# Optimization experiments

Hardware: AMD Instinct MI355X
Metric: run time of the kernel (lower is better)

Reference implementation:

```python
import jax, jax.numpy as jnp
import numpy as np

NUM_CODES = 8192
DIM = 256
TAU = 1.0
KL_WEIGHT = 0.01
COMMIT_WEIGHT = 0.25
B, C, P = 8, 64, 32


def setup_inputs() -> dict:
    key = jax.random.key(0)
    kz, kc = jax.random.split(key)
    z = jax.random.normal(kz, (B, C, P, DIM), dtype=jnp.float32)
    # nn.init.normal_(codebook.weight, std=1/sqrt(dim))
    codebook = jax.random.normal(kc, (NUM_CODES, DIM), dtype=jnp.float32) / jnp.sqrt(jnp.float32(DIM))
    return {"z": z, "codebook": codebook}


def reference(z, codebook):
    Bq, Cq, Pq, D = z.shape
    flat = z.reshape(-1, D)                                  # (N, D)
    logits = flat @ codebook.T                               # (N, num_codes)
    # training path: gumbel-softmax (hard=False), fixed key for determinism
    g = jax.random.gumbel(jax.random.key(42), logits.shape, dtype=logits.dtype)
    soft_one_hot = jax.nn.softmax((logits + g) / TAU, axis=-1)
    z_q = (soft_one_hot @ codebook).reshape(Bq, Cq, Pq, D)
    # KL to uniform prior: sum(qy * log(qy * K + 1e-10))
    log_qy = jax.nn.log_softmax(logits, axis=-1)
    qy = jnp.exp(log_qy)
    kl_loss = KL_WEIGHT * jnp.mean(jnp.sum(qy * jnp.log(qy * NUM_CODES + 1e-10), axis=-1))
    codes = jnp.argmax(logits, axis=-1).reshape(Bq, Cq, Pq)
    commit_loss = COMMIT_WEIGHT * jnp.mean((jax.lax.stop_gradient(z_q) - z) ** 2)
    z_q_st = z + jax.lax.stop_gradient(z_q - z)              # straight-through
    total_loss = commit_loss + kl_loss
    return (z_q_st, total_loss, codes)
```

## Files before the change

kernel.cpp:

```cpp
#include <hip/hip_runtime.h>
#include <stdint.h>
#include <math.h>

#define N_ROWS   16384
#define N_CODES  8192
#define DIMV     256
#define RT       32
#define CK       32
#define NCHUNK   (N_CODES / CK)
#define OUT_ZQ_N ((size_t)N_ROWS * DIMV)
#define OUT_LOSS OUT_ZQ_N
#define OUT_CODE (OUT_ZQ_N + 1)

#define WS_CBHI 0u
#define WS_CBT  4194304u
#define WS_ACC  8388608u
#define WS_NEED (8388608u + 64u)

#define CB1H_OFF  0
#define CBT_OFF   16896
#define BSTRIDE   1056
#define P_OFF     33792
#define P_ROW     80
#define S2B_OFF   36352
#define SKL_OFF   36608
#define TKL_OFF   36864
#define SMEM_BYTES 37120
#define ZT_ROWF   260
#define CAND_OFF  0

typedef __attribute__((ext_vector_type(8))) short short8;
typedef __attribute__((ext_vector_type(4))) float float4v;

typedef __attribute__((address_space(1))) uint32_t g_u32;
typedef __attribute__((address_space(3))) uint32_t l_u32;

__device__ __forceinline__ void dma16(const void* gsrc, void* ldst) {
  __builtin_amdgcn_global_load_lds((g_u32*)gsrc, (l_u32*)ldst, 16, 0, 0);
}

__device__ __forceinline__ uint32_t rotl32(uint32_t x, int r) {
  return __builtin_rotateleft32(x, (uint32_t)r);
}

__device__ __forceinline__ uint32_t threefry_bits(uint32_t c) {
  const uint32_t k0 = 0u, k1 = 42u;
  const uint32_t k2 = 0x1BD11BDAu ^ k0 ^ k1;
  uint32_t x0 = 0u + k0;
  uint32_t x1 = c + k1;
#define TF_R(r) { x0 += x1; x1 = rotl32(x1, r); x1 ^= x0; }
  TF_R(13) TF_R(15) TF_R(26) TF_R(6)
  x0 += k1; x1 += k2 + 1u;
  TF_R(17) TF_R(29) TF_R(16) TF_R(24)
  x0 += k2; x1 += k0 + 2u;
  TF_R(13) TF_R(15) TF_R(26) TF_R(6)
  x0 += k0; x1 += k1 + 3u;
  TF_R(17) TF_R(29) TF_R(16) TF_R(24)
  x0 += k1; x1 += k2 + 4u;
  TF_R(13) TF_R(15) TF_R(26) TF_R(6)
  x0 += k2; x1 += k0 + 5u;
#undef TF_R
  return x0 ^ x1;
}

__device__ __forceinline__ float gumbel_at_v1(uint32_t idx) {
  uint32_t bits = threefry_bits(idx);
  float u = __uint_as_float((bits >> 9) | 0x3f800000u) - 1.0f;
  u = fmaxf(u, 1.17549435e-38f);
  return -logf(-logf(u));
}

__device__ __forceinline__ unsigned short f2bf(float x) {
  uint32_t u = __float_as_uint(x);
  u += 0x7fffu + ((u >> 16) & 1u);
  return (unsigned short)(u >> 16);
}
__device__ __forceinline__ float bf2f(unsigned short h) {
  return __uint_as_float(((uint32_t)h) << 16);
}

__global__ __launch_bounds__(256)
void vq_prep(const float* __restrict__ cb, char* __restrict__ ws) {
  __shared__ unsigned short lhs[32 * 260];
  const int c = blockIdx.x;
  const int tid = threadIdx.x;
  const int k0 = c * 32;
  unsigned short* cbhi = (unsigned short*)(ws + WS_CBHI);
  unsigned short* cbt  = (unsigned short*)(ws + WS_CBT);
#pragma unroll
  for (int i = 0; i < 8; ++i) {
    int F = tid + i * 256;
    int code = F >> 6, d4 = (F & 63) * 4;
    float4 v = *(const float4*)(cb + (size_t)(k0 + code) * DIMV + d4);
    unsigned short h0 = f2bf(v.x), h1 = f2bf(v.y), h2 = f2bf(v.z), h3 = f2bf(v.w);
    ushort4 hv = {h0, h1, h2, h3};
    *(ushort4*)(cbhi + (size_t)(k0 + code) * DIMV + d4) = hv;
    *(ushort4*)(&lhs[code * 260 + d4]) = hv;
  }
  __syncthreads();
  const int d = tid;
  unsigned short vals[32];
#pragma unroll
  for (int cc = 0; cc < 32; ++cc) vals[cc] = lhs[cc * 260 + d];
  unsigned short* base = cbt + (size_t)c * 8192 + (size_t)d * 32;
#pragma unroll
  for (int j = 0; j < 8; ++j) {
    ushort4 w = {vals[4 * j], vals[4 * j + 1], vals[4 * j + 2], vals[4 * j + 3]};
    *(ushort4*)(base + j * 4) = w;
  }
}

__global__ __launch_bounds__(256, 4)
void vq_main_v2(const float* __restrict__ z, const float* __restrict__ cb,
                float* __restrict__ out, char* __restrict__ ws) {
  __shared__ __align__(16) char sm[SMEM_BYTES];
  const int tid  = threadIdx.x;
  const int wave = tid >> 6;
  const int lane = tid & 63;
  const int quad = lane >> 4;
  const int n    = lane & 15;
  const int mt   = wave & 1;
  const int nt   = wave >> 1;
  const int r0   = blockIdx.x * RT;
  const int myrow = mt * 16 + quad * 4;
  const char* cbhi_b = ws + WS_CBHI;
  const char* cbt_b  = ws + WS_CBT;
  float* wsA = (float*)(ws + WS_ACC);

  {
    float* zts = (float*)sm;
#pragma unroll
    for (int i = 0; i < 8; ++i) {
      int F = tid + i * 256;
      int row = F >> 6, d4 = (F & 63) * 4;
      *(float4*)(zts + row * ZT_ROWF + d4) =
          *(const float4*)(z + (size_t)(r0 + row) * DIMV + d4);
    }
  }
  __syncthreads();
  short8 zhi[8];
  {
    const float* zts = (const float*)sm;
    const int rowl = mt * 16 + n;
#pragma unroll
    for (int ks = 0; ks < 8; ++ks) {
      const float* zp = zts + rowl * ZT_ROWF + ks * 32 + quad * 8;
      float4 f0 = *(const float4*)zp;
      float4 f1 = *(const float4*)(zp + 4);
      zhi[ks][0] = (short)f2bf(f0.x); zhi[ks][1] = (short)f2bf(f0.y);
      zhi[ks][2] = (short)f2bf(f0.z); zhi[ks][3] = (short)f2bf(f0.w);
      zhi[ks][4] = (short)f2bf(f1.x); zhi[ks][5] = (short)f2bf(f1.y);
      zhi[ks][6] = (short)f2bf(f1.z); zhi[ks][7] = (short)f2bf(f1.w);
    }
  }
  __syncthreads();

#pragma unroll
  for (int i = 0; i < 4; ++i) {
    int b = wave * 4 + i;
    dma16(cbhi_b + (size_t)(2 * b) * 512 + (size_t)lane * 16, sm + CB1H_OFF + b * BSTRIDE);
  }

  float skl[4] = {0.f, 0.f, 0.f, 0.f};
  float tkl[4] = {0.f, 0.f, 0.f, 0.f};
  float s2l[4] = {0.f, 0.f, 0.f, 0.f};
  float v1[4], v2[4];
  int   i1[4], i2[4];
  uint32_t idxr[4];
#pragma unroll
  for (int r = 0; r < 4; ++r) {
    v1[r] = -INFINITY; v2[r] = -INFINITY;
    i1[r] = 0x7fffffff; i2[r] = 0x7fffffff;
    idxr[r] = (uint32_t)(r0 + myrow + r) * (uint32_t)N_CODES + (uint32_t)(nt * 16 + n);
  }
  float4v acc2[8];
#pragma unroll
  for (int t = 0; t < 8; ++t) acc2[t] = (float4v){0.f, 0.f, 0.f, 0.f};

  const int kc = nt * 16 + n;
  const char* bbase = sm + CB1H_OFF + (kc >> 1) * BSTRIDE + (kc & 1) * 512 + quad * 16;

  for (int c = 0; c < NCHUNK; ++c) {
    __syncthreads();

#pragma unroll
    for (int i = 0; i < 4; ++i) {
      int b = wave * 4 + i;
      dma16(cbt_b + (size_t)c * 16384 + (size_t)b * 1024 + (size_t)lane * 16,
            sm + CBT_OFF + b * BSTRIDE);
    }

    float4v e0 = (float4v){0.f, 0.f, 0.f, 0.f};
    float4v e1 = (float4v){0.f, 0.f, 0.f, 0.f};
#pragma unroll
    for (int ks = 0; ks < 4; ++ks) {
      short8 ba = *(const short8*)(bbase + (2 * ks) * 64);
      short8 bb = *(const short8*)(bbase + (2 * ks + 1) * 64);
      e0 = __builtin_amdgcn_mfma_f32_16x16x32_bf16(zhi[2 * ks], ba, e0, 0, 0, 0);
      e1 = __builtin_amdgcn_mfma_f32_16x16x32_bf16(zhi[2 * ks + 1], bb, e1, 0, 0, 0);
    }
    float4v acc1 = e0 + e1;

    const int codeg0 = c * CK + kc;
#pragma unroll
    for (int r = 0; r < 4; ++r) {
      float l = acc1[r];
      uint32_t bits = threefry_bits(idxr[r]);
      idxr[r] += 32u;
      float u = __uint_as_float((bits >> 9) | 0x3f800000u) - 1.0f;
      float t = -0.69314718056f * __log2f(fmaxf(u, 1.17549435e-38f));
      t = fmaxf(t, 1.0e-10f);
      float e = __expf(l);
      skl[r] += e;
      tkl[r] = fmaf(e, l, tkl[r]);
      bool b1 = l > v1[r];
      bool b2 = l > v2[r];
      v2[r] = b1 ? v1[r] : (b2 ? l : v2[r]);
      i2[r] = b1 ? i1[r] : (b2 ? codeg0 : i2[r]);
      v1[r] = b1 ? l : v1[r];
      i1[r] = b1 ? codeg0 : i1[r];
      float p = e * __builtin_amdgcn_rcpf(t) * 6.1442123533282097e-06f;
      unsigned short ph = f2bf(p);
      s2l[r] += bf2f(ph);
      *(unsigned short*)(sm + P_OFF + (myrow + r) * P_ROW + kc * 2) = ph;
    }
    __syncthreads();

    if (c + 1 < NCHUNK) {
      const size_t k1 = (size_t)(c + 1) * CK;
#pragma unroll
      for (int i = 0; i < 4; ++i) {
        int b = wave * 4 + i;
        dma16(cbhi_b + (k1 + 2 * b) * 512 + (size_t)lane * 16, sm + CB1H_OFF + b * BSTRIDE);
      }
    }

    {
      short8 pah0 = *(const short8*)(sm + P_OFF + n * P_ROW + quad * 16);
      short8 pah1 = *(const short8*)(sm + P_OFF + (16 + n) * P_ROW + quad * 16);
#pragma unroll
      for (int t = 0; t < 4; ++t) {
        int dt = wave * 4 + t;
        short8 bb = *(const short8*)(sm + CBT_OFF + dt * BSTRIDE + n * 64 + quad * 16);
        acc2[t * 2 + 0] = __builtin_amdgcn_mfma_f32_16x16x32_bf16(pah0, bb, acc2[t * 2 + 0], 0, 0, 0);
        acc2[t * 2 + 1] = __builtin_amdgcn_mfma_f32_16x16x32_bf16(pah1, bb, acc2[t * 2 + 1], 0, 0, 0);
      }
    }
  }

#pragma unroll
  for (int m = 1; m <= 8; m <<= 1) {
#pragma unroll
    for (int r = 0; r < 4; ++r) {
      s2l[r] += __shfl_xor(s2l[r], m);
      skl[r] += __shfl_xor(skl[r], m);
      tkl[r] += __shfl_xor(tkl[r], m);
    }
  }
  if (n == 0) {
    int off = (nt * 32 + myrow) * 4;
    float4 fs = {s2l[0], s2l[1], s2l[2], s2l[3]};
    *(float4*)(sm + S2B_OFF + off) = fs;
    float4 fk = {skl[0], skl[1], skl[2], skl[3]};
    *(float4*)(sm + SKL_OFF + off) = fk;
    float4 ft = {tkl[0], tkl[1], tkl[2], tkl[3]};
    *(float4*)(sm + TKL_OFF + off) = ft;
  }
#pragma unroll
  for (int r = 0; r < 4; ++r) {
    char* cbase = sm + CAND_OFF + (myrow + r) * 512 + (nt * 32 + n * 2) * 8;
    *(float*)(cbase + 0) = v1[r];
    *(int*)(cbase + 4)   = i1[r];
    *(float*)(cbase + 8) = v2[r];
    *(int*)(cbase + 12)  = i2[r];
  }
  __syncthreads();

  if (tid < 32) {
    int r = tid;
    const float* sklb = (const float*)(sm + SKL_OFF);
    const float* tklb = (const float*)(sm + TKL_OFF);
    float S = sklb[r] + sklb[32 + r];
    float T = tklb[r] + tklb[32 + r];
    float klr = T / S - __logf(S) + 9.010913347279288f;
#pragma unroll
    for (int m = 1; m <= 16; m <<= 1) klr += __shfl_xor(klr, m);
    if (r == 0) atomicAdd(&wsA[0], klr);
  }

  if (tid < 64) {
    int r = tid >> 1, h = tid & 1;
    const char* cbase = sm + CAND_OFF + r * 512 + h * 256;
    float bv[8]; int bi8[8];
#pragma unroll
    for (int k = 0; k < 8; ++k) { bv[k] = -INFINITY; bi8[k] = 0x7fffffff; }
    for (int s = 0; s < 32; ++s) {
      float v = *(const float*)(cbase + s * 8);
      int  id = *(const int*)(cbase + s * 8 + 4);
      if ((v > bv[7]) || (v == bv[7] && id < bi8[7])) {
        float cv = v; int ci = id;
#pragma unroll
        for (int k = 0; k < 8; ++k) {
          bool sw = (cv > bv[k]) || (cv == bv[k] && ci < bi8[k]);
          float tv = bv[k]; int ti = bi8[k];
          if (sw) { bv[k] = cv; bi8[k] = ci; cv = tv; ci = ti; }
        }
      }
    }
    float ovv[8]; int ovi[8];
#pragma unroll
    for (int k = 0; k < 8; ++k) {
      ovv[k] = __shfl_xor(bv[k], 1);
      ovi[k] = __shfl_xor(bi8[k], 1);
    }
#pragma unroll
    for (int kk = 0; kk < 8; ++kk) {
      float cv = ovv[kk]; int ci = ovi[kk];
      if ((cv > bv[7]) || (cv == bv[7] && ci < bi8[7])) {
#pragma unroll
        for (int k = 0; k < 8; ++k) {
          bool sw = (cv > bv[k]) || (cv == bv[k] && ci < bi8[k]);
          float tv = bv[k]; int ti = bi8[k];
          if (sw) { bv[k] = cv; bi8[k] = ci; cv = tv; ci = ti; }
        }
      }
    }
    const float* zp = z + (size_t)(r0 + r) * DIMV;
    double best = -1.0e300;
    int bidx = 0x7fffffff;
#pragma unroll
    for (int k = 0; k < 4; ++k) {
      int cidx = bi8[h * 4 + k];
      const float* cp = cb + (size_t)cidx * DIMV;
      double d = 0.0;
      for (int dd = 0; dd < DIMV; dd += 4) {
        float4 zv = *(const float4*)(zp + dd);
        float4 xv = *(const float4*)(cp + dd);
        d += (double)zv.x * xv.x + (double)zv.y * xv.y +
             (double)zv.z * xv.z + (double)zv.w * xv.w;
      }
      if (d > best || (d == best && cidx < bidx)) { best = d; bidx = cidx; }
    }
    double obest = __shfl_xor(best, 1);
    int    obidx = __shfl_xor(bidx, 1);
    bool take = (obest > best) || (obest == best && obidx < bidx);
    int finali = take ? obidx : bidx;
    if (h == 0) out[OUT_CODE + (size_t)(r0 + r)] = (float)finali;
  }

  float invm0[4], invm1[4];
  {
    const float* s2b = (const float*)(sm + S2B_OFF);
#pragma unroll
    for (int e = 0; e < 4; ++e) {
      float Sa = s2b[quad * 4 + e] + s2b[32 + quad * 4 + e];
      float Sb = s2b[16 + quad * 4 + e] + s2b[32 + 16 + quad * 4 + e];
      invm0[e] = 1.0f / Sa;
      invm1[e] = 1.0f / Sb;
    }
  }
  float cpart = 0.f;
#pragma unroll
  for (int t = 0; t < 4; ++t) {
    int dim = (wave * 4 + t) * 16 + n;
#pragma unroll
    for (int ms = 0; ms < 2; ++ms) {
      float4v a = acc2[t * 2 + ms];
#pragma unroll
      for (int e = 0; e < 4; ++e) {
        int row = ms * 16 + quad * 4 + e;
        float q = a[e] * (ms ? invm1[e] : invm0[e]);
        float zv = z[(size_t)(r0 + row) * DIMV + dim];
        float err = q - zv;
        cpart += err * err;
        out[(size_t)(r0 + row) * DIMV + dim] = zv + err;
      }
    }
  }
#pragma unroll
  for (int m = 1; m <= 32; m <<= 1) cpart += __shfl_xor(cpart, m);
  if (lane == 0) atomicAdd(&wsA[1], cpart);
}

#define ZSTRIDE  260
#define CSTRIDE  260
#define PSTRIDE  36
#define RSTRIDE  17

__global__ __launch_bounds__(256, 2)
void vq_main_v1(const float* __restrict__ z, const float* __restrict__ cb,
                float* __restrict__ out, float* __restrict__ ws_acc) {
  __shared__ float zt[RT * ZSTRIDE];
  __shared__ float cbt[CK * CSTRIDE];
  __shared__ float ptile[RT * PSTRIDE];
  __shared__ float redb[RT * RSTRIDE];
  __shared__ float m2s[RT], s2s[RT], scls[RT];

  const int tid = threadIdx.x;
  const int r0  = blockIdx.x * RT;
#pragma unroll
  for (int p = 0; p < 8; ++p) {
    int q = tid + p * 256;
    int i = q >> 6, c4 = (q & 63) * 4;
    *(float4*)(&zt[i * ZSTRIDE + c4]) = *(const float4*)(z + (size_t)(r0 + i) * DIMV + c4);
  }
  if (tid < RT) { m2s[tid] = -INFINITY; s2s[tid] = 0.f; scls[tid] = 0.f; }
  const int tr = tid & 15, tk = tid >> 4, rowg = tid >> 6;
  const int d4 = (tid & 63) * 4;
  float c_m[2][2], c_s[2][2], c_t[2][2];
  int   c_i[2][2];
#pragma unroll
  for (int a = 0; a < 2; ++a)
#pragma unroll
    for (int b = 0; b < 2; ++b) { c_m[a][b] = -INFINITY; c_s[a][b] = 0.f; c_t[a][b] = 0.f; c_i[a][b] = 0; }
  float acc2[8][4];
#pragma unroll
  for (int j = 0; j < 8; ++j)
#pragma unroll
    for (int e = 0; e < 4; ++e) acc2[j][e] = 0.f;
  __syncthreads();
  for (int c = 0; c < NCHUNK; ++c) {
    const int k0 = c * CK;
#pragma unroll
    for (int p = 0; p < 8; ++p) {
      int q = tid + p * 256;
      int i = q >> 6, c4 = (q & 63) * 4;
      *(float4*)(&cbt[i * CSTRIDE + c4]) = *(const float4*)(cb + (size_t)(k0 + i) * DIMV + c4);
    }
    __syncthreads();
    float l00 = 0.f, l01 = 0.f, l10 = 0.f, l11 = 0.f;
    {
      const float* zp0 = &zt[tr * ZSTRIDE];
      const float* zp1 = &zt[(tr + 16) * ZSTRIDE];
      const float* bp0 = &cbt[tk * CSTRIDE];
      const float* bp1 = &cbt[(tk + 16) * CSTRIDE];
#pragma unroll 4
      for (int d = 0; d < DIMV; d += 4) {
        float4 a0 = *(const float4*)(zp0 + d);
        float4 a1 = *(const float4*)(zp1 + d);
        float4 b0 = *(const float4*)(bp0 + d);
        float4 b1 = *(const float4*)(bp1 + d);
        l00 += a0.x*b0.x + a0.y*b0.y + a0.z*b0.z + a0.w*b0.w;
        l01 += a0.x*b1.x + a0.y*b1.y + a0.z*b1.z + a0.w*b1.w;
        l10 += a1.x*b0.x + a1.y*b0.y + a1.z*b0.z + a1.w*b0.w;
        l11 += a1.x*b1.x + a1.y*b1.y + a1.z*b1.z + a1.w*b1.w;
      }
    }
    float lv2[2][2] = {{l00, l01}, {l10, l11}};
    float a2[2][2];
#pragma unroll
    for (int a = 0; a < 2; ++a) {
      int grow = r0 + tr + a * 16;
#pragma unroll
      for (int b = 0; b < 2; ++b) {
        int gk = k0 + tk + b * 16;
        float g  = gumbel_at_v1((uint32_t)grow * (uint32_t)N_CODES + (uint32_t)gk);
        float lv = lv2[a][b];
        a2[a][b] = lv + g;
        if (lv > c_m[a][b]) {
          float sc = expf(c_m[a][b] - lv);
          c_s[a][b] = c_s[a][b] * sc + 1.0f;
          c_t[a][b] = c_t[a][b] * sc + lv;
          c_m[a][b] = lv;
          c_i[a][b] = gk;
        } else {
          float e = expf(lv - c_m[a][b]);
          c_s[a][b] += e;
          c_t[a][b] += e * lv;
        }
      }
    }
    redb[tr * RSTRIDE + tk]        = fmaxf(a2[0][0], a2[0][1]);
    redb[(tr + 16) * RSTRIDE + tk] = fmaxf(a2[1][0], a2[1][1]);
    __syncthreads();
    if (tid < RT) {
      float cm = -INFINITY;
#pragma unroll
      for (int j = 0; j < 16; ++j) cm = fmaxf(cm, redb[tid * RSTRIDE + j]);
      float m2n = fmaxf(m2s[tid], cm);
      scls[tid] = expf(m2s[tid] - m2n);
      m2s[tid]  = m2n;
    }
    __syncthreads();
#pragma unroll
    for (int a = 0; a < 2; ++a) {
      int row = tr + a * 16;
      float m2r = m2s[row];
      float p0 = expf(a2[a][0] - m2r);
      float p1 = expf(a2[a][1] - m2r);
      ptile[row * PSTRIDE + tk]      = p0;
      ptile[row * PSTRIDE + tk + 16] = p1;
      redb[row * RSTRIDE + tk] = p0 + p1;
    }
    __syncthreads();
    if (tid < RT) {
      float ss = 0.f;
#pragma unroll
      for (int j = 0; j < 16; ++j) ss += redb[tid * RSTRIDE + j];
      s2s[tid] = s2s[tid] * scls[tid] + ss;
    }
#pragma unroll
    for (int j = 0; j < 8; ++j) {
      float sc = scls[rowg * 8 + j];
      acc2[j][0] *= sc; acc2[j][1] *= sc; acc2[j][2] *= sc; acc2[j][3] *= sc;
    }
    for (int k4 = 0; k4 < CK; k4 += 4) {
      float4 cb0 = *(const float4*)(&cbt[(k4 + 0) * CSTRIDE + d4]);
      float4 cb1v = *(const float4*)(&cbt[(k4 + 1) * CSTRIDE + d4]);
      float4 cb2 = *(const float4*)(&cbt[(k4 + 2) * CSTRIDE + d4]);
      float4 cb3 = *(const float4*)(&cbt[(k4 + 3) * CSTRIDE + d4]);
#pragma unroll
      for (int j = 0; j < 8; ++j) {
        float4 p4 = *(const float4*)(&ptile[(rowg * 8 + j) * PSTRIDE + k4]);
        acc2[j][0] += p4.x*cb0.x + p4.y*cb1v.x + p4.z*cb2.x + p4.w*cb3.x;
        acc2[j][1] += p4.x*cb0.y + p4.y*cb1v.y + p4.z*cb2.y + p4.w*cb3.y;
        acc2[j][2] += p4.x*cb0.z + p4.y*cb1v.z + p4.z*cb2.z + p4.w*cb3.z;
        acc2[j][3] += p4.x*cb0.w + p4.y*cb1v.w + p4.z*cb2.w + p4.w*cb3.w;
      }
    }
    __syncthreads();
  }
  float* kbuf = cbt;
#pragma unroll
  for (int a = 0; a < 2; ++a) {
    float m0 = c_m[a][0], m1v = c_m[a][1];
    float m, s, t; int bi;
    if (m0 >= m1v) {
      float e = expf(m1v - m0);
      m = m0; s = c_s[a][0] + c_s[a][1] * e; t = c_t[a][0] + c_t[a][1] * e;
    } else {
      float e = expf(m0 - m1v);
      m = m1v; s = c_s[a][0] * e + c_s[a][1]; t = c_t[a][0] * e + c_t[a][1];
    }
    if (m0 > m1v)      bi = c_i[a][0];
    else if (m1v > m0) bi = c_i[a][1];
    else               bi = min(c_i[a][0], c_i[a][1]);
    int row = tr + a * 16;
    kbuf[row * 65 + tk * 4 + 0] = m;
    kbuf[row * 65 + tk * 4 + 1] = s;
    kbuf[row * 65 + tk * 4 + 2] = t;
    kbuf[row * 65 + tk * 4 + 3] = (float)bi;
  }
  __syncthreads();
  if (tid < RT) {
    int r = tid;
    float M = -INFINITY, S = 0.f, T = 0.f, BM = -INFINITY;
    int BI = 0x7fffffff;
    for (int j = 0; j < 16; ++j) {
      float m  = kbuf[r * 65 + j * 4 + 0];
      float s  = kbuf[r * 65 + j * 4 + 1];
      float t  = kbuf[r * 65 + j * 4 + 2];
      int   bi = (int)kbuf[r * 65 + j * 4 + 3];
      if (m <= M) {
        float e = expf(m - M);
        S += s * e; T += t * e;
      } else {
        float e = expf(M - m);
        S = S * e + s; T = T * e + t; M = m;
      }
      if (m > BM || (m == BM && bi < BI)) { BM = m; BI = bi; }
    }
    float kl = logf((float)N_CODES) + T / S - M - logf(S);
    atomicAdd(&ws_acc[0], kl);
    out[OUT_CODE + (size_t)(r0 + r)] = (float)BI;
  }
  float cpart = 0.f;
#pragma unroll
  for (int j = 0; j < 8; ++j) {
    int row  = rowg * 8 + j;
    int grow = r0 + row;
    float inv = 1.0f / s2s[row];
    float4 zv = *(const float4*)(&zt[row * ZSTRIDE + d4]);
    float q0 = acc2[j][0] * inv, q1 = acc2[j][1] * inv;
    float q2 = acc2[j][2] * inv, q3 = acc2[j][3] * inv;
    float e0 = q0 - zv.x, e1 = q1 - zv.y, e2 = q2 - zv.z, e3 = q3 - zv.w;
    cpart += e0*e0 + e1*e1 + e2*e2 + e3*e3;
    float4 o;
    o.x = zv.x + e0; o.y = zv.y + e1; o.z = zv.z + e2; o.w = zv.w + e3;
    *(float4*)(&out[(size_t)grow * DIMV + d4]) = o;
  }
#pragma unroll
  for (int off = 32; off > 0; off >>= 1) cpart += __shfl_down(cpart, off, 64);
  __syncthreads();
  if ((tid & 63) == 0) redb[tid >> 6] = cpart;
  __syncthreads();
  if (tid == 0) {
    float cs = redb[0] + redb[1] + redb[2] + redb[3];
    atomicAdd(&ws_acc[1], cs);
  }
}

__global__ void vq_finalize(const float* __restrict__ ws_acc, float* __restrict__ out) {
  if (threadIdx.x == 0 && blockIdx.x == 0) {
    float kl = 0.01f * (ws_acc[0] / (float)N_ROWS);
    float cm = 0.25f * (ws_acc[1] / (float)OUT_ZQ_N);
    out[OUT_LOSS] = cm + kl;
  }
}

extern "C" void kernel_launch(void* const* d_in, const int* in_sizes, int n_in,
                              void* d_out, int out_size, void* d_ws, size_t ws_size,
                              hipStream_t stream) {
  (void)in_sizes; (void)n_in; (void)out_size;
  const float* z  = (const float*)d_in[0];
  const float* cb = (const float*)d_in[1];
  float* out = (float*)d_out;
  if (ws_size >= (size_t)WS_NEED) {
    char* ws = (char*)d_ws;
    hipMemsetAsync(ws + WS_ACC, 0, 8, stream);
    vq_prep<<<256, 256, 0, stream>>>(cb, ws);
    vq_main_v2<<<N_ROWS / RT, 256, 0, stream>>>(z, cb, out, ws);
    vq_finalize<<<1, 64, 0, stream>>>((const float*)(ws + WS_ACC), out);
  } else {
    float* ws = (float*)d_ws;
    hipMemsetAsync(ws, 0, 8, stream);
    vq_main_v1<<<N_ROWS / RT, 256, 0, stream>>>(z, cb, out, ws);
    vq_finalize<<<1, 64, 0, stream>>>(ws, out);
  }
}
```

Before: 706.7 us.

## Double code chunk to 64 with 512-thread blocks and read transposed codebook from global

The main kernel now runs 8 waves per block and processes 64 codes per iteration instead of 32, which halves the number of loop iterations and block-wide barriers. The second GEMM (soft one-hot times codebook) no longer stages the transposed codebook tile in LDS via DMA. Each wave instead loads its B fragments straight from global memory into registers, covering 32 output dims. Partial sums and candidate buffers are widened to four code groups. The trade-offs are higher register pressure, exposed global-load latency inside the loop, and a longer serial top-8 candidate merge.

```diff
diff --git a/kernel.cpp b/kernel.cpp
--- a/kernel.cpp
+++ b/kernel.cpp
@@ -8,6 +8,8 @@
 #define RT       32
 #define CK       32
 #define NCHUNK   (N_CODES / CK)
+#define CK2      64
+#define NITER    (N_CODES / CK2)
 #define OUT_ZQ_N ((size_t)N_ROWS * DIMV)
 #define OUT_LOSS OUT_ZQ_N
 #define OUT_CODE (OUT_ZQ_N + 1)
@@ -18,14 +20,13 @@
 #define WS_NEED (8388608u + 64u)
 
 #define CB1H_OFF  0
-#define CBT_OFF   16896
 #define BSTRIDE   1056
 #define P_OFF     33792
-#define P_ROW     80
-#define S2B_OFF   36352
-#define SKL_OFF   36608
-#define TKL_OFF   36864
-#define SMEM_BYTES 37120
+#define P_ROW     144
+#define S2B_OFF   38400
+#define SKL_OFF   38912
+#define TKL_OFF   39424
+#define SMEM_BYTES 39936
 #define ZT_ROWF   260
 #define CAND_OFF  0
 
@@ -110,8 +111,8 @@
   }
 }
 
-__global__ __launch_bounds__(256, 4)
-void vq_main_v2(const float* __restrict__ z, const float* __restrict__ cb,
+__global__ __launch_bounds__(512, 4)
+void vq_main_v3(const float* __restrict__ z, const float* __restrict__ cb,
                 float* __restrict__ out, char* __restrict__ ws) {
   __shared__ __align__(16) char sm[SMEM_BYTES];
   const int tid  = threadIdx.x;
@@ -130,8 +131,8 @@
   {
     float* zts = (float*)sm;
 #pragma unroll
-    for (int i = 0; i < 8; ++i) {
-      int F = tid + i * 256;
+    for (int i = 0; i < 4; ++i) {
+      int F = tid + i * 512;
       int row = F >> 6, d4 = (F & 63) * 4;
       *(float4*)(zts + row * ZT_ROWF + d4) =
           *(const float4*)(z + (size_t)(r0 + row) * DIMV + d4);
@@ -166,47 +167,45 @@
   float s2l[4] = {0.f, 0.f, 0.f, 0.f};
   float v1[4], v2[4];
   int   i1[4], i2[4];
-  uint32_t idxr[4];
 #pragma unroll
   for (int r = 0; r < 4; ++r) {
     v1[r] = -INFINITY; v2[r] = -INFINITY;
     i1[r] = 0x7fffffff; i2[r] = 0x7fffffff;
-    idxr[r] = (uint32_t)(r0 + myrow + r) * (uint32_t)N_CODES + (uint32_t)(nt * 16 + n);
-  }
-  float4v acc2[8];
-#pragma unroll
-  for (int t = 0; t < 8; ++t) acc2[t] = (float4v){0.f, 0.f, 0.f, 0.f};
-
+  }
   const int kc = nt * 16 + n;
+  uint32_t idxA = (uint32_t)(r0 + myrow) * (uint32_t)N_CODES + (uint32_t)kc;
+  float4v acc2[4];
+#pragma unroll
+  for (int t = 0; t < 4; ++t) acc2[t] = (float4v){0.f, 0.f, 0.f, 0.f};
+
   const char* bbase = sm + CB1H_OFF + (kc >> 1) * BSTRIDE + (kc & 1) * 512 + quad * 16;
-
-  for (int c = 0; c < NCHUNK; ++c) {
+  const char* g2base = cbt_b + ((size_t)(wave * 32 + n) * 32 + (size_t)(quad * 8)) * 2;
+
+  for (int c = 0; c < NITER; ++c) {
     __syncthreads();
 
-#pragma unroll
-    for (int i = 0; i < 4; ++i) {
-      int b = wave * 4 + i;
-      dma16(cbt_b + (size_t)c * 16384 + (size_t)b * 1024 + (size_t)lane * 16,
-            sm + CBT_OFF + b * BSTRIDE);
-    }
+    const char* gc = g2base + (size_t)(2 * c) * 16384;
+    short8 bb00 = *(const short8*)(gc);
+    short8 bb01 = *(const short8*)(gc + 1024);
+    short8 bb10 = *(const short8*)(gc + 16384);
+    short8 bb11 = *(const short8*)(gc + 16384 + 1024);
 
     float4v e0 = (float4v){0.f, 0.f, 0.f, 0.f};
     float4v e1 = (float4v){0.f, 0.f, 0.f, 0.f};
 #pragma unroll
     for (int ks = 0; ks < 4; ++ks) {
-      short8 ba = *(const short8*)(bbase + (2 * ks) * 64);
-      short8 bb = *(const short8*)(bbase + (2 * ks + 1) * 64);
+      short8 ba  = *(const short8*)(bbase + (2 * ks) * 64);
+      short8 bbv = *(const short8*)(bbase + (2 * ks + 1) * 64);
       e0 = __builtin_amdgcn_mfma_f32_16x16x32_bf16(zhi[2 * ks], ba, e0, 0, 0, 0);
-      e1 = __builtin_amdgcn_mfma_f32_16x16x32_bf16(zhi[2 * ks + 1], bb, e1, 0, 0, 0);
+      e1 = __builtin_amdgcn_mfma_f32_16x16x32_bf16(zhi[2 * ks + 1], bbv, e1, 0, 0, 0);
     }
     float4v acc1 = e0 + e1;
 
-    const int codeg0 = c * CK + kc;
+    const int codeg0 = c * CK2 + kc;
 #pragma unroll
     for (int r = 0; r < 4; ++r) {
       float l = acc1[r];
-      uint32_t bits = threefry_bits(idxr[r]);
-      idxr[r] += 32u;
+      uint32_t bits = threefry_bits(idxA + (uint32_t)r * (uint32_t)N_CODES);
       float u = __uint_as_float((bits >> 9) | 0x3f800000u) - 1.0f;
       float t = -0.69314718056f * __log2f(fmaxf(u, 1.17549435e-38f));
       t = fmaxf(t, 1.0e-10f);
@@ -224,10 +223,11 @@
       s2l[r] += bf2f(ph);
       *(unsigned short*)(sm + P_OFF + (myrow + r) * P_ROW + kc * 2) = ph;
     }
+    idxA += (uint32_t)CK2;
     __syncthreads();
 
-    if (c + 1 < NCHUNK) {
-      const size_t k1 = (size_t)(c + 1) * CK;
+    if (c + 1 < NITER) {
+      const size_t k1 = (size_t)(c + 1) * CK2;
 #pragma unroll
       for (int i = 0; i < 4; ++i) {
         int b = wave * 4 + i;
@@ -236,15 +236,18 @@
     }
 
     {
-      short8 pah0 = *(const short8*)(sm + P_OFF + n * P_ROW + quad * 16);
-      short8 pah1 = *(const short8*)(sm + P_OFF + (16 + n) * P_ROW + quad * 16);
-#pragma unroll
-      for (int t = 0; t < 4; ++t) {
-        int dt = wave * 4 + t;
-        short8 bb = *(const short8*)(sm + CBT_OFF + dt * BSTRIDE + n * 64 + quad * 16);
-        acc2[t * 2 + 0] = __builtin_amdgcn_mfma_f32_16x16x32_bf16(pah0, bb, acc2[t * 2 + 0], 0, 0, 0);
-        acc2[t * 2 + 1] = __builtin_amdgcn_mfma_f32_16x16x32_bf16(pah1, bb, acc2[t * 2 + 1], 0, 0, 0);
-      }
+      short8 pa00 = *(const short8*)(sm + P_OFF + n * P_ROW + quad * 16);
+      short8 pa01 = *(const short8*)(sm + P_OFF + n * P_ROW + 64 + quad * 16);
+      short8 pa10 = *(const short8*)(sm + P_OFF + (16 + n) * P_ROW + quad * 16);
+      short8 pa11 = *(const short8*)(sm + P_OFF + (16 + n) * P_ROW + 64 + quad * 16);
+      acc2[0] = __builtin_amdgcn_mfma_f32_16x16x32_bf16(pa00, bb00, acc2[0], 0, 0, 0);
+      acc2[0] = __builtin_amdgcn_mfma_f32_16x16x32_bf16(pa01, bb10, acc2[0], 0, 0, 0);
+      acc2[1] = __builtin_amdgcn_mfma_f32_16x16x32_bf16(pa00, bb01, acc2[1], 0, 0, 0);
+      acc2[1] = __builtin_amdgcn_mfma_f32_16x16x32_bf16(pa01, bb11, acc2[1], 0, 0, 0);
+      acc2[2] = __builtin_amdgcn_mfma_f32_16x16x32_bf16(pa10, bb00, acc2[2], 0, 0, 0);
+      acc2[2] = __builtin_amdgcn_mfma_f32_16x16x32_bf16(pa11, bb10, acc2[2], 0, 0, 0);
+      acc2[3] = __builtin_amdgcn_mfma_f32_16x16x32_bf16(pa10, bb01, acc2[3], 0, 0, 0);
+      acc2[3] = __builtin_amdgcn_mfma_f32_16x16x32_bf16(pa11, bb11, acc2[3], 0, 0, 0);
     }
   }
 
@@ -258,7 +261,7 @@
     }
   }
   if (n == 0) {
-    int off = (nt * 32 + myrow) * 4;
+    int off = nt * 128 + myrow * 4;
     float4 fs = {s2l[0], s2l[1], s2l[2], s2l[3]};
     *(float4*)(sm + S2B_OFF + off) = fs;
     float4 fk = {skl[0], skl[1], skl[2], skl[3]};
@@ -268,7 +271,7 @@
   }
 #pragma unroll
   for (int r = 0; r < 4; ++r) {
-    char* cbase = sm + CAND_OFF + (myrow + r) * 512 + (nt * 32 + n * 2) * 8;
+    char* cbase = sm + CAND_OFF + (myrow + r) * 1024 + kc * 16;
     *(float*)(cbase + 0) = v1[r];
     *(int*)(cbase + 4)   = i1[r];
     *(float*)(cbase + 8) = v2[r];
@@ -280,8 +283,8 @@
     int r = tid;
     const float* sklb = (const float*)(sm + SKL_OFF);
     const float* tklb = (const float*)(sm + TKL_OFF);
-    float S = sklb[r] + sklb[32 + r];
-    float T = tklb[r] + tklb[32 + r];
+    float S = (sklb[r] + sklb[32 + r]) + (sklb[64 + r] + sklb[96 + r]);
+    float T = (tklb[r] + tklb[32 + r]) + (tklb[64 + r] + tklb[96 + r]);
     float klr = T / S - __logf(S) + 9.010913347279288f;
 #pragma unroll
     for (int m = 1; m <= 16; m <<= 1) klr += __shfl_xor(klr, m);
@@ -290,11 +293,11 @@
 
   if (tid < 64) {
     int r = tid >> 1, h = tid & 1;
-    const char* cbase = sm + CAND_OFF + r * 512 + h * 256;
+    const char* cbase = sm + CAND_OFF + r * 1024 + h * 512;
     float bv[8]; int bi8[8];
 #pragma unroll
     for (int k = 0; k < 8; ++k) { bv[k] = -INFINITY; bi8[k] = 0x7fffffff; }
-    for (int s = 0; s < 32; ++s) {
+    for (int s = 0; s < 64; ++s) {
       float v = *(const float*)(cbase + s * 8);
       int  id = *(const int*)(cbase + s * 8 + 4);
       if ((v > bv[7]) || (v == bv[7] && id < bi8[7])) {
@@ -353,19 +356,20 @@
     const float* s2b = (const float*)(sm + S2B_OFF);
 #pragma unroll
     for (int e = 0; e < 4; ++e) {
-      float Sa = s2b[quad * 4 + e] + s2b[32 + quad * 4 + e];
-      float Sb = s2b[16 + quad * 4 + e] + s2b[32 + 16 + quad * 4 + e];
+      int ra = quad * 4 + e, rb = 16 + quad * 4 + e;
+      float Sa = (s2b[ra] + s2b[32 + ra]) + (s2b[64 + ra] + s2b[96 + ra]);
+      float Sb = (s2b[rb] + s2b[32 + rb]) + (s2b[64 + rb] + s2b[96 + rb]);
       invm0[e] = 1.0f / Sa;
       invm1[e] = 1.0f / Sb;
     }
   }
   float cpart = 0.f;
 #pragma unroll
-  for (int t = 0; t < 4; ++t) {
-    int dim = (wave * 4 + t) * 16 + n;
+  for (int t = 0; t < 2; ++t) {
+    int dim = wave * 32 + t * 16 + n;
 #pragma unroll
     for (int ms = 0; ms < 2; ++ms) {
-      float4v a = acc2[t * 2 + ms];
+      float4v a = acc2[ms * 2 + t];
 #pragma unroll
       for (int e = 0; e < 4; ++e) {
         int row = ms * 16 + quad * 4 + e;
@@ -609,7 +613,7 @@
     char* ws = (char*)d_ws;
     hipMemsetAsync(ws + WS_ACC, 0, 8, stream);
     vq_prep<<<256, 256, 0, stream>>>(cb, ws);
-    vq_main_v2<<<N_ROWS / RT, 256, 0, stream>>>(z, cb, out, ws);
+    vq_main_v3<<<N_ROWS / RT, 512, 0, stream>>>(z, cb, out, ws);
     vq_finalize<<<1, 64, 0, stream>>>((const float*)(ws + WS_ACC), out);
   } else {
     float* ws = (float*)d_ws;
```

Result: faster. 674.9 us (-4.5%).
